# Optimization experiments

Hardware: AMD Instinct MI355X
Metric: run time of the kernel (lower is better)

The kernel has to match this reference:

```python
import math
import jax, jax.numpy as jnp
import numpy as np

B, W_LEN, C = 4, 2048, 768
H = 3  # fixed number of heads in the module
K = C // H  # head dim


def setup_inputs() -> dict:
    key = jax.random.key(0)
    k1, k2, k3 = jax.random.split(key, 3)
    in_sequence_bwc = jax.random.normal(k1, (B, W_LEN, C), dtype=jnp.float32)
    # torch nn.Linear weights: [out_features, in_features], scaled for stability
    W_qkv = jax.random.normal(k2, (3 * C, C), dtype=jnp.float32) * (1.0 / math.sqrt(C))
    W_proj = jax.random.normal(k3, (C, C), dtype=jnp.float32) * (1.0 / math.sqrt(C))
    return {"in_sequence_bwc": in_sequence_bwc, "W_qkv": W_qkv, "W_proj": W_proj}


def reference(in_sequence_bwc, W_qkv, W_proj):
    batch, words, coords = in_sequence_bwc.shape
    head_dim = coords // H
    # qkv projection: x @ W^T  -> [b, w, 3c]
    all_bwd = jnp.einsum("bwc,dc->bwd", in_sequence_bwc, W_qkv)
    q_bwc, k_bwc, v_bwc = jnp.split(all_bwd, 3, axis=-1)
    # [b, h, w, k]
    q = q_bwc.reshape(batch, words, H, head_dim).transpose(0, 2, 1, 3)
    k = k_bwc.reshape(batch, words, H, head_dim).transpose(0, 2, 1, 3)
    v = v_bwc.reshape(batch, words, H, head_dim).transpose(0, 2, 1, 3)
    # scaled scores with causal mask -> softmax -> @V
    scores = jnp.einsum("bhqk,bhmk->bhqm", q, k) / math.sqrt(head_dim)
    causal = jnp.tril(jnp.ones((words, words), dtype=bool))
    scores = jnp.where(causal[None, None], scores, -jnp.inf)
    probs = jax.nn.softmax(scores, axis=-1)
    out = jnp.einsum("bhqm,bhmk->bhqk", probs, v)
    out_bwc = out.transpose(0, 2, 1, 3).reshape(batch, words, coords)
    return jnp.einsum("bwc,dc->bwd", out_bwc, W_proj)
```

## Files before the change

### kernel.cpp

```cpp
#include <hip/hip_runtime.h>

using v8h = __attribute__((ext_vector_type(8))) _Float16;
using v4f = __attribute__((ext_vector_type(4))) float;
using v4u = __attribute__((ext_vector_type(4))) unsigned short;
using v8u = __attribute__((ext_vector_type(8))) unsigned short;

__device__ __forceinline__ unsigned short f2h(float x) {
  _Float16 h = (_Float16)x;
  return __builtin_bit_cast(unsigned short, h);
}
__device__ __forceinline__ float h2f(unsigned short u) {
  return (float)__builtin_bit_cast(_Float16, u);
}

__device__ __forceinline__ void gl_lds16(const unsigned short* g, unsigned short* l) {
  __builtin_amdgcn_global_load_lds(
      (const __attribute__((address_space(1))) unsigned int*)g,
      (__attribute__((address_space(3))) unsigned int*)l, 16, 0, 0);
}

__global__ void cvt_kernel(const float* __restrict__ src,
                           unsigned short* __restrict__ dst, int n8) {
  int i = blockIdx.x * 256 + threadIdx.x;
  if (i >= n8) return;
  const float* p = src + (size_t)i * 8;
  float4 a = *(const float4*)p;
  float4 b = *(const float4*)(p + 4);
  v8u o = {f2h(a.x), f2h(a.y), f2h(a.z), f2h(a.w),
           f2h(b.x), f2h(b.y), f2h(b.z), f2h(b.w)};
  *(v8u*)(dst + (size_t)i * 8) = o;
}

template <int MODE, bool OF>
__global__ __launch_bounds__(256, 2)
void gemm_async_kernel(const unsigned short* __restrict__ A,
                       const unsigned short* __restrict__ Bw,
                       void* __restrict__ Cv, unsigned short* __restrict__ VT,
                       int K, int ldc) {
  __shared__ unsigned short As[4096];
  __shared__ unsigned short Bs[4096];

  const int t    = threadIdx.x;
  const int ln   = t & 63;
  const int wv   = t >> 6;
  const int quad = ln >> 4;
  const int L    = ln & 15;
  const int wm   = (wv >> 1) * 64;
  const int wn   = (wv & 1) * 64;
  const long m0  = (long)blockIdx.y * 128;
  const long n0  = (long)blockIdx.x * 128;

  v4f acc[4][4];
#pragma unroll
  for (int i = 0; i < 4; i++)
#pragma unroll
    for (int j = 0; j < 4; j++) acc[i][j] = (v4f){0.f, 0.f, 0.f, 0.f};

  const int ar = t >> 2;
  const int ac = (t & 3) * 8;
  const unsigned short* Ag = A + (m0 + ar) * (long)K + ac;
  const unsigned short* Bg = Bw + (n0 + ar) * (long)K + ac;
  unsigned short* la = &As[t * 8];
  unsigned short* lb = &Bs[t * 8];
  const long rowskip = 64L * K;

  for (int k0 = 0; k0 < K; k0 += 32) {
    gl_lds16(Ag + k0, la);
    gl_lds16(Ag + rowskip + k0, la + 2048);
    gl_lds16(Bg + k0, lb);
    gl_lds16(Bg + rowskip + k0, lb + 2048);
    __syncthreads();

    v8h af[4], bfr[4];
#pragma unroll
    for (int i = 0; i < 4; i++)
      af[i] = *(const v8h*)(&As[(wm + i * 16 + L) * 32 + quad * 8]);
#pragma unroll
    for (int j = 0; j < 4; j++)
      bfr[j] = *(const v8h*)(&Bs[(wn + j * 16 + L) * 32 + quad * 8]);
#pragma unroll
    for (int i = 0; i < 4; i++)
#pragma unroll
      for (int j = 0; j < 4; j++)
        acc[i][j] = __builtin_amdgcn_mfma_f32_16x16x32_f16(af[i], bfr[j], acc[i][j], 0, 0, 0);
    __syncthreads();
  }

  if (MODE == 0 || n0 < 1536) {
#pragma unroll
    for (int i = 0; i < 4; i++)
#pragma unroll
      for (int j = 0; j < 4; j++)
#pragma unroll
        for (int r = 0; r < 4; r++) {
          long row = m0 + wm + i * 16 + quad * 4 + r;
          long col = n0 + wn + j * 16 + L;
          if (OF) ((float*)Cv)[row * ldc + col] = acc[i][j][r];
          else    ((unsigned short*)Cv)[row * ldc + col] = f2h(acc[i][j][r]);
        }
  } else {
#pragma unroll
    for (int i = 0; i < 4; i++)
#pragma unroll
      for (int j = 0; j < 4; j++) {
        int colp   = (int)(n0 + wn + j * 16 + L) - 1536;
        int h      = colp >> 8;
        int d      = colp & 255;
        long token = m0 + wm + i * 16 + quad * 4;
        int b  = (int)(token >> 11);
        int tk = (int)(token & 2047);
        v4u val = {f2h(acc[i][j][0]), f2h(acc[i][j][1]), f2h(acc[i][j][2]), f2h(acc[i][j][3])};
        *(v4u*)(&VT[((long)(b * 3 + h) * 256 + d) * 2048 + tk]) = val;
      }
  }
}

__global__ __launch_bounds__(256, 2)
void gemm_sc_kernel(const unsigned short* __restrict__ QK,
                    unsigned short* __restrict__ Sc) {
  __shared__ unsigned short As[4096];
  __shared__ unsigned short Bs[4096];

  const int t    = threadIdx.x;
  const int ln   = t & 63;
  const int wv   = t >> 6;
  const int quad = ln >> 4;
  const int L    = ln & 15;
  const int wm   = (wv >> 1) * 64;
  const int wn   = (wv & 1) * 64;

  int x = (int)blockIdx.x, i = 0;
  while (x >= i + 1) { x -= i + 1; i++; }
  const int j  = x;
  const int bh = (int)blockIdx.y;
  const int b  = bh / 3, h = bh % 3;
  const long tokA = (long)b * 2048 + i * 128;
  const long tokB = (long)b * 2048 + j * 128;

  v4f acc[4][4];
#pragma unroll
  for (int ii = 0; ii < 4; ii++)
#pragma unroll
    for (int jj = 0; jj < 4; jj++) acc[ii][jj] = (v4f){0.f, 0.f, 0.f, 0.f};

  const int ar = t >> 2;
  const int ac = (t & 3) * 8;
  const unsigned short* Ag = QK + (tokA + ar) * 1536 + h * 256 + ac;
  const unsigned short* Bg = QK + (tokB + ar) * 1536 + 768 + h * 256 + ac;
  unsigned short* la = &As[t * 8];
  unsigned short* lb = &Bs[t * 8];
  const long rowskip = 64L * 1536;

  for (int k0 = 0; k0 < 256; k0 += 32) {
    gl_lds16(Ag + k0, la);
    gl_lds16(Ag + rowskip + k0, la + 2048);
    gl_lds16(Bg + k0, lb);
    gl_lds16(Bg + rowskip + k0, lb + 2048);
    __syncthreads();

    v8h af[4], bfr[4];
#pragma unroll
    for (int ii = 0; ii < 4; ii++)
      af[ii] = *(const v8h*)(&As[(wm + ii * 16 + L) * 32 + quad * 8]);
#pragma unroll
    for (int jj = 0; jj < 4; jj++)
      bfr[jj] = *(const v8h*)(&Bs[(wn + jj * 16 + L) * 32 + quad * 8]);
#pragma unroll
    for (int ii = 0; ii < 4; ii++)
#pragma unroll
      for (int jj = 0; jj < 4; jj++)
        acc[ii][jj] = __builtin_amdgcn_mfma_f32_16x16x32_f16(af[ii], bfr[jj], acc[ii][jj], 0, 0, 0);
    __syncthreads();
  }

  unsigned short* Sb = Sc + ((long)bh * 136 + blockIdx.x) * 16384;
#pragma unroll
  for (int ii = 0; ii < 4; ii++)
#pragma unroll
    for (int jj = 0; jj < 4; jj++)
#pragma unroll
      for (int r = 0; r < 4; r++) {
        int row = wm + ii * 16 + quad * 4 + r;
        int col = wn + jj * 16 + L;
        Sb[row * 128 + col] = f2h(acc[ii][jj][r]);
      }
}

__global__ __launch_bounds__(256, 4)
void softmax_kernel(unsigned short* __restrict__ Sc) {
  const int tt   = threadIdx.x;
  const int wv   = tt >> 6;
  const int lane = tt & 63;
  const int bh   = (int)blockIdx.y;

  const int r = 2047 - ((int)blockIdx.x * 4 + wv);
  const int i = r >> 7;
  const int rowloc = r & 127;
  const long base = ((long)bh * 136 + (long)i * (i + 1) / 2) * 16384 + rowloc * 128;
  const int Lrow = (i + 1) * 128;
  const int nch = (i + 4) >> 2;

  float xs[4][8];
  float mx = -1e30f;
  for (int k = 0; k < nch; k++) {
    int c0 = k * 512 + lane * 8;
    if (c0 < Lrow) {
      int j = c0 >> 7;
      v8u v = *(const v8u*)(Sc + base + (long)j * 16384 + (c0 & 127));
#pragma unroll
      for (int e = 0; e < 8; e++) {
        float f = (c0 + e <= r) ? h2f(v[e]) * 0.0625f : -1e30f;
        xs[k][e] = f;
        mx = fmaxf(mx, f);
      }
    } else {
#pragma unroll
      for (int e = 0; e < 8; e++) xs[k][e] = -1e30f;
    }
  }
#pragma unroll
  for (int d = 1; d < 64; d <<= 1) mx = fmaxf(mx, __shfl_xor(mx, d));

  float sum = 0.f;
  for (int k = 0; k < nch; k++)
#pragma unroll
    for (int e = 0; e < 8; e++) {
      float ex = __expf(xs[k][e] - mx);
      xs[k][e] = ex;
      sum += ex;
    }
#pragma unroll
  for (int d = 1; d < 64; d <<= 1) sum += __shfl_xor(sum, d);
  const float inv = 1.0f / sum;

  for (int k = 0; k < nch; k++) {
    int c0 = k * 512 + lane * 8;
    if (c0 < Lrow) {
      int j = c0 >> 7;
      v8u o;
#pragma unroll
      for (int e = 0; e < 8; e++) o[e] = f2h(xs[k][e] * inv);
      *(v8u*)(Sc + base + (long)j * 16384 + (c0 & 127)) = o;
    }
  }
}

__global__ __launch_bounds__(256, 2)
void gemm_pv_kernel(const unsigned short* __restrict__ Sc,
                    const unsigned short* __restrict__ VT,
                    unsigned short* __restrict__ Pp) {
  __shared__ unsigned short As[4096];
  __shared__ unsigned short Bs[4096];

  const int t    = threadIdx.x;
  const int ln   = t & 63;
  const int wv   = t >> 6;
  const int quad = ln >> 4;
  const int L    = ln & 15;
  const int wm   = (wv >> 1) * 64;
  const int wn   = (wv & 1) * 64;

  const int ix  = (int)blockIdx.x;
  const int i   = 15 - (ix >> 2);
  const int nh  = (ix >> 1) & 1;
  const int par = ix & 1;
  const int bh  = (int)blockIdx.y;

  v4f acc[4][4];
#pragma unroll
  for (int ii = 0; ii < 4; ii++)
#pragma unroll
    for (int jj = 0; jj < 4; jj++) acc[ii][jj] = (v4f){0.f, 0.f, 0.f, 0.f};

  const int ar = t >> 2;
  const int ac = (t & 3) * 8;
  const unsigned short* Abase =
      Sc + ((long)bh * 136 + (long)i * (i + 1) / 2) * 16384 + ar * 128 + ac;
  const unsigned short* Bg =
      VT + ((long)bh * 256 + nh * 128 + ar) * 2048 + ac;
  unsigned short* la = &As[t * 8];
  unsigned short* lb = &Bs[t * 8];

  for (int j = par; j <= i; j += 2) {
    const unsigned short* Aj = Abase + (long)j * 16384;
    const unsigned short* Bj = Bg + j * 128;
#pragma unroll
    for (int k0 = 0; k0 < 128; k0 += 32) {
      gl_lds16(Aj + k0, la);
      gl_lds16(Aj + 64 * 128 + k0, la + 2048);
      gl_lds16(Bj + k0, lb);
      gl_lds16(Bj + 64 * 2048 + k0, lb + 2048);
      __syncthreads();

      v8h af[4], bfr[4];
#pragma unroll
      for (int ii = 0; ii < 4; ii++)
        af[ii] = *(const v8h*)(&As[(wm + ii * 16 + L) * 32 + quad * 8]);
#pragma unroll
      for (int jj = 0; jj < 4; jj++)
        bfr[jj] = *(const v8h*)(&Bs[(wn + jj * 16 + L) * 32 + quad * 8]);
#pragma unroll
      for (int ii = 0; ii < 4; ii++)
#pragma unroll
        for (int jj = 0; jj < 4; jj++)
          acc[ii][jj] = __builtin_amdgcn_mfma_f32_16x16x32_f16(af[ii], bfr[jj], acc[ii][jj], 0, 0, 0);
      __syncthreads();
    }
  }

  unsigned short* Pb = Pp + ((((long)bh * 16 + i) * 2 + nh) * 2 + par) * 16384;
#pragma unroll
  for (int ii = 0; ii < 4; ii++)
#pragma unroll
    for (int jj = 0; jj < 4; jj++)
#pragma unroll
      for (int r = 0; r < 4; r++) {
        int row = wm + ii * 16 + quad * 4 + r;
        int col = wn + jj * 16 + L;
        Pb[row * 128 + col] = f2h(acc[ii][jj][r]);
      }
}

__global__ __launch_bounds__(256, 4)
void pv_combine_kernel(const unsigned short* __restrict__ Pp,
                       unsigned short* __restrict__ AO) {
  const int i  = (int)blockIdx.x >> 1;
  const int nh = (int)blockIdx.x & 1;
  const int bh = (int)blockIdx.y;
  const int b  = bh / 3, h = bh % 3;

  const int tid = threadIdx.x;
  const int row = tid >> 1;
  const int cs  = (tid & 1) * 64;

  const unsigned short* P0 = Pp + ((((long)bh * 16 + i) * 2 + nh) * 2 + 0) * 16384 + row * 128 + cs;
  const unsigned short* P1 = P0 + 16384;
  unsigned short* Or = AO + ((long)b * 2048 + i * 128 + row) * 768 + h * 256 + nh * 128 + cs;
#pragma unroll
  for (int q = 0; q < 8; q++) {
    v8u a = *(const v8u*)(P0 + q * 8);
    v8u c = *(const v8u*)(P1 + q * 8);
    v8u o;
#pragma unroll
    for (int e = 0; e < 8; e++) o[e] = f2h(h2f(a[e]) + h2f(c[e]));
    *(v8u*)(Or + q * 8) = o;
  }
}

extern "C" void kernel_launch(void* const* d_in, const int* in_sizes, int n_in,
                              void* d_out, int out_size, void* d_ws, size_t ws_size,
                              hipStream_t stream) {
  const float* X     = (const float*)d_in[0];
  const float* Wqkv  = (const float*)d_in[1];
  const float* Wproj = (const float*)d_in[2];
  float* out = (float*)d_out;

  const size_t SZ_QK = (size_t)8192 * 1536 * 2;
  const size_t SZ_VT = (size_t)3072 * 2048 * 2;
  const size_t SZ_SC = (size_t)12 * 136 * 16384 * 2;
  const size_t SZ_AO = (size_t)8192 * 768 * 2;
  const size_t SZ_WQ = (size_t)2304 * 768 * 2;

  char* ws = (char*)d_ws;
  unsigned short* QKb = (unsigned short*)ws;
  unsigned short* Ppb = QKb;
  unsigned short* VTb = (unsigned short*)(ws + SZ_QK);
  unsigned short* Scb = (unsigned short*)(ws + SZ_QK + SZ_VT);
  unsigned short* Xb  = Scb;
  unsigned short* AOb = (unsigned short*)(ws + SZ_QK + SZ_VT + SZ_SC);
  unsigned short* Wqb = (unsigned short*)(ws + SZ_QK + SZ_VT + SZ_SC + SZ_AO);
  unsigned short* Wpb = (unsigned short*)(ws + SZ_QK + SZ_VT + SZ_SC + SZ_AO + SZ_WQ);

  dim3 blk(256, 1, 1);
  cvt_kernel<<<dim3(3072, 1, 1), blk, 0, stream>>>(X, Xb, 786432);
  cvt_kernel<<<dim3(864, 1, 1), blk, 0, stream>>>(Wqkv, Wqb, 221184);
  cvt_kernel<<<dim3(288, 1, 1), blk, 0, stream>>>(Wproj, Wpb, 73728);
  gemm_async_kernel<1, false><<<dim3(18, 64, 1), blk, 0, stream>>>(
      Xb, Wqb, QKb, VTb, 768, 1536);
  gemm_sc_kernel<<<dim3(136, 12, 1), blk, 0, stream>>>(QKb, Scb);
  softmax_kernel<<<dim3(512, 12, 1), blk, 0, stream>>>(Scb);
  gemm_pv_kernel<<<dim3(64, 12, 1), blk, 0, stream>>>(Scb, VTb, Ppb);
  pv_combine_kernel<<<dim3(32, 12, 1), blk, 0, stream>>>(Ppb, AOb);
  gemm_async_kernel<0, true><<<dim3(6, 64, 1), blk, 0, stream>>>(
      AOb, Wpb, out, (unsigned short*)nullptr, 768, 768);
}
```

Measured before the change: 260.4 us.

## Replace QKV projection GEMM with 256x256-tile 8-wave ping-pong pipelined kernel

Adds a dedicated QKV projection kernel that uses 512 threads and 256x256 output tiles. It double-buffers LDS through async global-to-LDS loads interleaved with four MFMA phases, and uses barriers plus s_setprio so memory and compute overlap across waves. Larger tiles raise reuse and cut global traffic, and the staggered pipeline is meant to hide load latency. The cost is 128KB of LDS per block and a grid of only 288 blocks, which risks low occupancy and poor CU fill.

Result: no change. 265.6 us (+2.0%).

```diff
diff --git a/kernel.cpp b/kernel.cpp
--- a/kernel.cpp
+++ b/kernel.cpp
@@ -31,6 +31,184 @@
   *(v8u*)(dst + (size_t)i * 8) = o;
 }
 
+__global__ __launch_bounds__(512, 2)
+void qkv8_kernel(const unsigned short* __restrict__ A,
+                 const unsigned short* __restrict__ Bw,
+                 unsigned short* __restrict__ QK,
+                 unsigned short* __restrict__ VT) {
+  __shared__ unsigned short sm[65536];
+  const int t    = (int)threadIdx.x;
+  const int ln   = t & 63;
+  const int wv   = t >> 6;
+  const int quad = ln >> 4;
+  const int L    = ln & 15;
+  const int wm   = wv >> 2;
+  const int wn   = wv & 3;
+  const long m0  = (long)blockIdx.y * 256;
+  const long n0  = (long)blockIdx.x * 256;
+
+  const int srow = t >> 3;
+  const int scol = ((t & 7) ^ (srow & 7)) * 8;
+  const unsigned short* Ath = A + (m0 + srow) * 768 + scol;
+  const unsigned short* Bth = Bw + (n0 + srow) * 768 + scol;
+  unsigned short* lth = &sm[t * 8];
+
+  const int l7   = L & 7;
+  const int sl0  = ((0 + quad) ^ l7) * 8;
+  const int sl1  = ((4 + quad) ^ l7) * 8;
+  const int arow = (wm * 128 + L) * 64;
+  const int brow = (wn * 64 + L) * 64;
+
+  v4f acc[8][4];
+#pragma unroll
+  for (int i = 0; i < 8; i++)
+#pragma unroll
+    for (int j = 0; j < 4; j++) acc[i][j] = (v4f){0.f, 0.f, 0.f, 0.f};
+
+  auto stA = [&](int tile, int h) {
+    if (tile >= 12) return;
+    const unsigned short* g = Ath + (h * 128) * 768 + tile * 64;
+    unsigned short* l = lth + (tile & 1) * 32768 + h * 8192;
+    gl_lds16(g, l);
+    gl_lds16(g + 64 * 768, l + 4096);
+  };
+  auto stB = [&](int tile, int h) {
+    if (tile >= 12) return;
+    const unsigned short* g = Bth + (h * 128) * 768 + tile * 64;
+    unsigned short* l = lth + (tile & 1) * 32768 + 16384 + h * 8192;
+    gl_lds16(g, l);
+    gl_lds16(g + 64 * 768, l + 4096);
+  };
+
+  stB(0, 0); stB(0, 1); stA(0, 0); stA(0, 1);
+  stB(1, 0); stB(1, 1); stA(1, 0);
+  asm volatile("s_waitcnt vmcnt(6)" ::: "memory");
+  __builtin_amdgcn_s_barrier();
+  __builtin_amdgcn_sched_barrier(0);
+
+#pragma unroll 2
+  for (int kt = 0; kt < 12; ++kt) {
+    const unsigned short* sA = &sm[(kt & 1) * 32768];
+    const unsigned short* sB = sA + 16384;
+    v8h af[4][2], b0[2][2], b1[2][2];
+
+#pragma unroll
+    for (int i = 0; i < 4; i++) {
+      af[i][0] = *(const v8h*)&sA[arow + i * 1024 + sl0];
+      af[i][1] = *(const v8h*)&sA[arow + i * 1024 + sl1];
+    }
+#pragma unroll
+    for (int j = 0; j < 2; j++) {
+      b0[j][0] = *(const v8h*)&sB[brow + j * 1024 + sl0];
+      b0[j][1] = *(const v8h*)&sB[brow + j * 1024 + sl1];
+    }
+    stA(kt + 1, 1);
+    __builtin_amdgcn_s_barrier();
+    asm volatile("s_waitcnt lgkmcnt(0)" ::: "memory");
+    __builtin_amdgcn_sched_barrier(0);
+    __builtin_amdgcn_s_setprio(1);
+#pragma unroll
+    for (int i = 0; i < 4; i++)
+#pragma unroll
+      for (int j = 0; j < 2; j++) {
+        acc[i][j] = __builtin_amdgcn_mfma_f32_16x16x32_f16(af[i][0], b0[j][0], acc[i][j], 0, 0, 0);
+        acc[i][j] = __builtin_amdgcn_mfma_f32_16x16x32_f16(af[i][1], b0[j][1], acc[i][j], 0, 0, 0);
+      }
+    __builtin_amdgcn_s_setprio(0);
+    __builtin_amdgcn_s_barrier();
+    __builtin_amdgcn_sched_barrier(0);
+
+#pragma unroll
+    for (int j = 0; j < 2; j++) {
+      b1[j][0] = *(const v8h*)&sB[brow + 2048 + j * 1024 + sl0];
+      b1[j][1] = *(const v8h*)&sB[brow + 2048 + j * 1024 + sl1];
+    }
+    __builtin_amdgcn_s_barrier();
+    asm volatile("s_waitcnt lgkmcnt(0)" ::: "memory");
+    __builtin_amdgcn_sched_barrier(0);
+    __builtin_amdgcn_s_setprio(1);
+#pragma unroll
+    for (int i = 0; i < 4; i++)
+#pragma unroll
+      for (int j = 0; j < 2; j++) {
+        acc[i][2 + j] = __builtin_amdgcn_mfma_f32_16x16x32_f16(af[i][0], b1[j][0], acc[i][2 + j], 0, 0, 0);
+        acc[i][2 + j] = __builtin_amdgcn_mfma_f32_16x16x32_f16(af[i][1], b1[j][1], acc[i][2 + j], 0, 0, 0);
+      }
+    __builtin_amdgcn_s_setprio(0);
+    __builtin_amdgcn_s_barrier();
+    __builtin_amdgcn_sched_barrier(0);
+
+#pragma unroll
+    for (int i = 0; i < 4; i++) {
+      af[i][0] = *(const v8h*)&sA[arow + 4096 + i * 1024 + sl0];
+      af[i][1] = *(const v8h*)&sA[arow + 4096 + i * 1024 + sl1];
+    }
+    stB(kt + 2, 0);
+    __builtin_amdgcn_s_barrier();
+    asm volatile("s_waitcnt lgkmcnt(0)" ::: "memory");
+    __builtin_amdgcn_sched_barrier(0);
+    __builtin_amdgcn_s_setprio(1);
+#pragma unroll
+    for (int i = 0; i < 4; i++)
+#pragma unroll
+      for (int j = 0; j < 2; j++) {
+        acc[4 + i][2 + j] = __builtin_amdgcn_mfma_f32_16x16x32_f16(af[i][0], b1[j][0], acc[4 + i][2 + j], 0, 0, 0);
+        acc[4 + i][2 + j] = __builtin_amdgcn_mfma_f32_16x16x32_f16(af[i][1], b1[j][1], acc[4 + i][2 + j], 0, 0, 0);
+      }
+    __builtin_amdgcn_s_setprio(0);
+    __builtin_amdgcn_s_barrier();
+    __builtin_amdgcn_sched_barrier(0);
+
+    stB(kt + 2, 1);
+    stA(kt + 2, 0);
+    __builtin_amdgcn_s_barrier();
+    __builtin_amdgcn_sched_barrier(0);
+    __builtin_amdgcn_s_setprio(1);
+#pragma unroll
+    for (int i = 0; i < 4; i++)
+#pragma unroll
+      for (int j = 0; j < 2; j++) {
+        acc[4 + i][j] = __builtin_amdgcn_mfma_f32_16x16x32_f16(af[i][0], b0[j][0], acc[4 + i][j], 0, 0, 0);
+        acc[4 + i][j] = __builtin_amdgcn_mfma_f32_16x16x32_f16(af[i][1], b0[j][1], acc[4 + i][j], 0, 0, 0);
+      }
+    __builtin_amdgcn_s_setprio(0);
+    if (kt + 2 < 12)      { asm volatile("s_waitcnt vmcnt(6)" ::: "memory"); }
+    else if (kt + 1 < 12) { asm volatile("s_waitcnt vmcnt(0)" ::: "memory"); }
+    __builtin_amdgcn_s_barrier();
+    __builtin_amdgcn_sched_barrier(0);
+  }
+
+  if (n0 < 1536) {
+#pragma unroll
+    for (int mi = 0; mi < 8; mi++) {
+      const long row = m0 + wm * 128 + (mi >> 2) * 64 + (mi & 3) * 16 + quad * 4;
+#pragma unroll
+      for (int nj = 0; nj < 4; nj++) {
+        const long col = n0 + wn * 64 + nj * 16 + L;
+#pragma unroll
+        for (int r = 0; r < 4; r++)
+          QK[(row + r) * 1536 + col] = f2h(acc[mi][nj][r]);
+      }
+    }
+  } else {
+#pragma unroll
+    for (int mi = 0; mi < 8; mi++) {
+      const long token = m0 + wm * 128 + (mi >> 2) * 64 + (mi & 3) * 16 + quad * 4;
+      const int b  = (int)(token >> 11);
+      const int tk = (int)(token & 2047);
+#pragma unroll
+      for (int nj = 0; nj < 4; nj++) {
+        const int colp = (int)(n0 + wn * 64 + nj * 16 + L) - 1536;
+        const int h = colp >> 8;
+        const int d = colp & 255;
+        v4u val = {f2h(acc[mi][nj][0]), f2h(acc[mi][nj][1]),
+                   f2h(acc[mi][nj][2]), f2h(acc[mi][nj][3])};
+        *(v4u*)(&VT[((long)(b * 3 + h) * 256 + d) * 2048 + tk]) = val;
+      }
+    }
+  }
+}
+
 template <int MODE, bool OF>
 __global__ __launch_bounds__(256, 2)
 void gemm_async_kernel(const unsigned short* __restrict__ A,
@@ -375,8 +553,7 @@
   cvt_kernel<<<dim3(3072, 1, 1), blk, 0, stream>>>(X, Xb, 786432);
   cvt_kernel<<<dim3(864, 1, 1), blk, 0, stream>>>(Wqkv, Wqb, 221184);
   cvt_kernel<<<dim3(288, 1, 1), blk, 0, stream>>>(Wproj, Wpb, 73728);
-  gemm_async_kernel<1, false><<<dim3(18, 64, 1), blk, 0, stream>>>(
-      Xb, Wqb, QKb, VTb, 768, 1536);
+  qkv8_kernel<<<dim3(9, 32, 1), dim3(512, 1, 1), 0, stream>>>(Xb, Wqb, QKb, VTb);
   gemm_sc_kernel<<<dim3(136, 12, 1), blk, 0, stream>>>(QKb, Scb);
   softmax_kernel<<<dim3(512, 12, 1), blk, 0, stream>>>(Scb);
   gemm_pv_kernel<<<dim3(64, 12, 1), blk, 0, stream>>>(Scb, VTb, Ppb);
```
